# Kernel optimization log

Hardware: AMD Instinct MI355X
Metric: run time of the kernel (lower is better)

Reference implementation:

```python
import jax, jax.numpy as jnp
import numpy as np

E = 16        # n_experts
K = 2         # n_active_experts
D = 2048      # d_model
F = 1408      # ffn_hidden
B, S = 4, 2048


def _swiglu(x, wg, wu, wd):
    # x: [N, D]; wg/wu: [F, D]; wd: [D, F]
    return (jax.nn.silu(x @ wg.T) * (x @ wu.T)) @ wd.T


def setup_inputs() -> dict:
    key = jax.random.key(0)
    ks = jax.random.split(key, 8)
    sc = 0.02
    return {
        "x": jax.random.normal(ks[0], (B, S, D), jnp.float32),
        "gate_w": jax.random.normal(ks[1], (E, D), jnp.float32) * sc,
        "w_gate": jax.random.normal(ks[2], (E, F, D), jnp.float32) * sc,
        "w_up": jax.random.normal(ks[3], (E, F, D), jnp.float32) * sc,
        "w_down": jax.random.normal(ks[4], (E, D, F), jnp.float32) * sc,
        "sw_gate": jax.random.normal(ks[5], (F, D), jnp.float32) * sc,
        "sw_up": jax.random.normal(ks[6], (F, D), jnp.float32) * sc,
        "sw_down": jax.random.normal(ks[7], (D, F), jnp.float32) * sc,
        "expert_bias": jnp.zeros((E,), jnp.float32),
    }


def reference(x, gate_w, w_gate, w_up, w_down, sw_gate, sw_up, sw_down, expert_bias):
    b, s, d = x.shape
    flat = x.reshape(-1, d)                           # [N, D]
    logits = flat @ gate_w.T                          # [N, E]
    probs = jax.nn.softmax(logits, axis=-1)
    biased = logits + expert_bias
    _, top_idx = jax.lax.top_k(biased, K)             # [N, K] int32
    top_w = jnp.take_along_axis(probs, top_idx, axis=-1)
    top_w = top_w / jnp.sum(top_w, axis=-1, keepdims=True)
    # scatter top-k weights into a dense per-expert combine matrix [N, E]
    combine = jnp.sum(jax.nn.one_hot(top_idx, E, dtype=flat.dtype) * top_w[..., None], axis=1)
    out = jnp.zeros_like(flat)
    for e in range(E):  # fixed small expert loop
        out = out + combine[:, e:e + 1] * _swiglu(flat, w_gate[e], w_up[e], w_down[e])
    out = out + _swiglu(flat, sw_gate, sw_up, sw_down)  # shared expert
    return out.reshape(b, s, d)
```

## Files before the change

### kernel.cpp

```cpp
#include <hip/hip_runtime.h>
#include <hip/hip_bf16.h>
#include <cstdint>

#define NE 16
#define D_ 2048
#define F_ 1408
#define NTOK 8192
#define NPAIR (NTOK * 2)
#define SHARED_BASE NPAIR
#define NTOT (NPAIR + NTOK)

#define BM1 256
#define BN1 128
#define BN2 256
#define BK 64
#define NF1 (F_ / BN1)
#define NF2 (D_ / BN2)
#define MAXRT 111

typedef __attribute__((ext_vector_type(8))) short short8;
typedef __attribute__((ext_vector_type(4))) float f32x4;

static __device__ __forceinline__ ushort f2bf(float f) {
    union { float f; unsigned u; } v; v.f = f;
    unsigned u = v.u;
    return (ushort)((u + 0x7FFFu + ((u >> 16) & 1u)) >> 16);
}

static __device__ __forceinline__ float bf2f(ushort u) {
    union { unsigned u; float f; } v; v.u = ((unsigned)u) << 16;
    return v.f;
}

static __device__ __forceinline__ void cvt_store8(ushort* dst, const float* src) {
    const float4* s = reinterpret_cast<const float4*>(src);
    float4 a = s[0], b = s[1];
    short8 v;
    v[0] = (short)f2bf(a.x); v[1] = (short)f2bf(a.y);
    v[2] = (short)f2bf(a.z); v[3] = (short)f2bf(a.w);
    v[4] = (short)f2bf(b.x); v[5] = (short)f2bf(b.y);
    v[6] = (short)f2bf(b.z); v[7] = (short)f2bf(b.w);
    *reinterpret_cast<short8*>(dst) = v;
}

static __device__ __forceinline__ void gll16(const void* g, void* l) {
    __builtin_amdgcn_global_load_lds((const __attribute__((address_space(1))) void*)g,
                                     (__attribute__((address_space(3))) void*)l, 16, 0, 0);
}

static __device__ __forceinline__ int xcd_map(int p, int nwg) {
    int q = nwg >> 3, r = nwg & 7;
    int x = p & 7, k = p >> 3;
    int base = (x < r) ? x * (q + 1) : r * (q + 1) + (x - r) * q;
    return base + k;
}

__global__ __launch_bounds__(256) void k_cvt(const float* __restrict__ src,
                                             ushort* __restrict__ dst, int n8) {
    int i = blockIdx.x * 256 + threadIdx.x;
    int stride = gridDim.x * 256;
    for (; i < n8; i += stride) cvt_store8(dst + (size_t)i * 8, src + (size_t)i * 8);
}

__global__ __launch_bounds__(256) void k_route(const float* __restrict__ x,
                                               const float* __restrict__ gate_w,
                                               const float* __restrict__ expert_bias,
                                               int* __restrict__ topk_idx,
                                               float* __restrict__ topk_w) {
    const int wave = threadIdx.x >> 6;
    const int lane = threadIdx.x & 63;
    const int tok = blockIdx.x * 4 + wave;
    if (tok >= NTOK) return;
    const float* xr = x + (size_t)tok * D_;
    float xv[D_ / 64];
#pragma unroll
    for (int i = 0; i < D_ / 64; ++i) xv[i] = xr[lane + 64 * i];

    float logits[NE];
#pragma unroll
    for (int e = 0; e < NE; ++e) {
        const float* gw = gate_w + e * D_;
        float p = 0.f;
#pragma unroll
        for (int i = 0; i < D_ / 64; ++i) p += xv[i] * gw[lane + 64 * i];
#pragma unroll
        for (int off = 32; off > 0; off >>= 1) p += __shfl_xor(p, off, 64);
        logits[e] = p;
    }
    int i1 = 0; float b1 = logits[0] + expert_bias[0];
#pragma unroll
    for (int e = 1; e < NE; ++e) {
        float b = logits[e] + expert_bias[e];
        if (b > b1) { b1 = b; i1 = e; }
    }
    int i2 = -1; float b2 = -3.4e38f;
#pragma unroll
    for (int e = 0; e < NE; ++e) {
        if (e == i1) continue;
        float b = logits[e] + expert_bias[e];
        if (b > b2) { b2 = b; i2 = e; }
    }
    float l1 = logits[i1], l2 = logits[i2];
    float m = fmaxf(l1, l2);
    float e1 = __expf(l1 - m), e2 = __expf(l2 - m);
    float s = e1 + e2;
    if (lane == 0) {
        topk_idx[tok * 2 + 0] = i1;
        topk_idx[tok * 2 + 1] = i2;
        topk_w[tok * 2 + 0] = e1 / s;
        topk_w[tok * 2 + 1] = e2 / s;
    }
}

__global__ void k_zero_meta(int* meta) {
    if (threadIdx.x < 128) meta[threadIdx.x] = 0;
}

__global__ __launch_bounds__(256) void k_count(const int* __restrict__ topk_idx,
                                               int* __restrict__ meta) {
    int t = blockIdx.x * 256 + threadIdx.x;
    if (t >= NTOK) return;
    atomicAdd(&meta[topk_idx[t * 2 + 0]], 1);
    atomicAdd(&meta[topk_idx[t * 2 + 1]], 1);
}

__global__ void k_prefix(int* meta) {
    if (threadIdx.x == 0) {
        int acc = 0;
        for (int e = 0; e < NE; ++e) { meta[32 + e] = acc; acc += meta[e]; }
        meta[32 + NE] = acc;
        int t = 0;
        for (int e = 0; e < NE; ++e) { meta[64 + e] = t; t += (meta[e] + BM1 - 1) / BM1; }
        meta[64 + NE] = t;
        meta[64 + NE + 1] = t + NTOK / BM1;
    }
}

__global__ __launch_bounds__(256) void k_scatter(const int* __restrict__ topk_idx,
                                                 const float* __restrict__ topk_w,
                                                 int* __restrict__ meta,
                                                 int* __restrict__ tok_sorted,
                                                 float* __restrict__ w_sorted,
                                                 int* __restrict__ inv) {
    int t = blockIdx.x * 256 + threadIdx.x;
    if (t >= NTOK) return;
#pragma unroll
    for (int k = 0; k < 2; ++k) {
        int e = topk_idx[t * 2 + k];
        int p = atomicAdd(&meta[16 + e], 1);
        int idx = meta[32 + e] + p;
        tok_sorted[idx] = t;
        w_sorted[idx] = topk_w[t * 2 + k];
        inv[t * 2 + k] = idx;
    }
}

static __device__ __forceinline__ bool grid_decode(const int* meta, int bid, int NF,
                                                   int& e, int& row0, int& fx) {
    if (bid >= meta[64 + NE + 1] * NF) return false;
    e = (bid >= meta[64 + NE] * NF) ? NE : 0;
    if (e == 0) {
#pragma unroll
        for (int i = 1; i < NE; ++i) if (bid >= meta[64 + i] * NF) e = i;
    }
    const int tile_base = meta[64 + e];
    const int nrt = meta[64 + e + 1] - tile_base;
    const int bw = bid - tile_base * NF;
    fx = bw / nrt;
    row0 = (bw - fx * nrt) * BM1;
    return true;
}

__global__ __launch_bounds__(512, 2) void k_ffn1(const ushort* __restrict__ xb,
                                                 const ushort* __restrict__ wgb,
                                                 const ushort* __restrict__ wub,
                                                 const ushort* __restrict__ swgb,
                                                 const ushort* __restrict__ swub,
                                                 const int* __restrict__ meta,
                                                 const int* __restrict__ tok_sorted,
                                                 const float* __restrict__ w_sorted,
                                                 ushort* __restrict__ Hbuf) {
    int e, row0, fx;
    const int lbid = xcd_map(blockIdx.x, gridDim.x);
    if (!grid_decode(meta, lbid, NF1, e, row0, fx)) return;
    int n_e, base;
    if (e < NE) { n_e = meta[e]; base = meta[32 + e]; }
    else        { n_e = NTOK;    base = SHARED_BASE; }
    const int f0 = fx * BN1;
    const ushort* wg = (e < NE) ? wgb + (size_t)e * F_ * D_ : swgb;
    const ushort* wu = (e < NE) ? wub + (size_t)e * F_ * D_ : swub;

    __shared__ __align__(16) ushort As[2][BM1 * BK];
    __shared__ __align__(16) ushort Gs[2][BN1 * BK];
    __shared__ __align__(16) ushort Us[2][BN1 * BK];
    __shared__ int tks[BM1];
    __shared__ float tws[BM1];

    const int tid = threadIdx.x;
    const int wv = tid >> 6, lane = tid & 63;
    if (tid < BM1) {
        int r = row0 + tid;
        if (r < n_e) {
            tks[tid] = (e < NE) ? tok_sorted[base + r] : r;
            tws[tid] = (e < NE) ? w_sorted[base + r] : 1.0f;
        } else { tks[tid] = 0; tws[tid] = 0.f; }
    }
    __syncthreads();

    const ushort* srcA[4]; const ushort* srcG[2]; const ushort* srcU[2];
#pragma unroll
    for (int j = 0; j < 4; ++j) {
        int c = j * 512 + wv * 64 + lane;
        int r = c >> 3;
        int col = ((c & 7) ^ (r & 7)) * 8;
        srcA[j] = xb + (size_t)tks[r] * D_ + col;
    }
#pragma unroll
    for (int j = 0; j < 2; ++j) {
        int c = j * 512 + wv * 64 + lane;
        int r = c >> 3;
        int col = ((c & 7) ^ (r & 7)) * 8;
        srcG[j] = wg + (size_t)(f0 + r) * D_ + col;
        srcU[j] = wu + (size_t)(f0 + r) * D_ + col;
    }

    auto stage = [&](int buf, int k0) {
        char* bA = (char*)(&As[buf][0]) + wv * 1024;
        char* bG = (char*)(&Gs[buf][0]) + wv * 1024;
        char* bU = (char*)(&Us[buf][0]) + wv * 1024;
        gll16(srcA[0] + k0, bA);         gll16(srcA[1] + k0, bA + 8192);
        gll16(srcA[2] + k0, bA + 16384); gll16(srcA[3] + k0, bA + 24576);
        gll16(srcG[0] + k0, bG);         gll16(srcG[1] + k0, bG + 8192);
        gll16(srcU[0] + k0, bU);         gll16(srcU[1] + k0, bU + 8192);
    };

    f32x4 accg[4][4] = {}; f32x4 accu[4][4] = {};
    const int wm = (wv >> 1) * 64, wn = (wv & 1) * 64;
    const int fr = lane & 15, fq = lane >> 4;
    const int sw = fr & 7;
    const int rc0 = ((fq ^ sw) * 8);
    const int rc1 = (((4 + fq) ^ sw) * 8);

    auto compute = [&](int buf) {
        const ushort* pA = As[buf];
        const ushort* pG = Gs[buf];
        const ushort* pU = Us[buf];
#pragma unroll
        for (int kk = 0; kk < 2; ++kk) {
            const int rc = kk ? rc1 : rc0;
            short8 af[4], gf[4], uf[4];
#pragma unroll
            for (int mi = 0; mi < 4; ++mi)
                af[mi] = *reinterpret_cast<const short8*>(&pA[(wm + mi * 16 + fr) * BK + rc]);
#pragma unroll
            for (int ni = 0; ni < 4; ++ni) {
                gf[ni] = *reinterpret_cast<const short8*>(&pG[(wn + ni * 16 + fr) * BK + rc]);
                uf[ni] = *reinterpret_cast<const short8*>(&pU[(wn + ni * 16 + fr) * BK + rc]);
            }
#pragma unroll
            for (int mi = 0; mi < 4; ++mi)
#pragma unroll
                for (int ni = 0; ni < 4; ++ni) {
                    accg[mi][ni] = __builtin_amdgcn_mfma_f32_16x16x32_bf16(af[mi], gf[ni], accg[mi][ni], 0, 0, 0);
                    accu[mi][ni] = __builtin_amdgcn_mfma_f32_16x16x32_bf16(af[mi], uf[ni], accu[mi][ni], 0, 0, 0);
                }
        }
    };

    const int NK = D_ / BK;
    stage(0, 0);
    stage(1, BK);
    asm volatile("s_waitcnt vmcnt(8)" ::: "memory");
    __builtin_amdgcn_s_barrier();
    __builtin_amdgcn_sched_barrier(0);
    int cur = 0;
    for (int ks = 0; ks < NK; ++ks) {
        compute(cur);
        __builtin_amdgcn_s_barrier();
        if (ks + 2 < NK) {
            stage(cur, (ks + 2) * BK);
            asm volatile("s_waitcnt vmcnt(8)" ::: "memory");
        } else if (ks + 1 < NK) {
            asm volatile("s_waitcnt vmcnt(0)" ::: "memory");
        }
        __builtin_amdgcn_s_barrier();
        __builtin_amdgcn_sched_barrier(0);
        cur ^= 1;
    }

#pragma unroll
    for (int mi = 0; mi < 4; ++mi) {
#pragma unroll
        for (int r = 0; r < 4; ++r) {
            int lr = wm + mi * 16 + fq * 4 + r;
            int grow = row0 + lr;
            if (grow < n_e) {
                float w = tws[lr];
                ushort* hrow = Hbuf + (size_t)(base + grow) * F_ + f0 + wn;
#pragma unroll
                for (int ni = 0; ni < 4; ++ni) {
                    float g = accg[mi][ni][r];
                    float u = accu[mi][ni][r];
                    float h = w * (g / (1.f + __expf(-g))) * u;
                    hrow[ni * 16 + fr] = f2bf(h);
                }
            }
        }
    }
}

__global__ __launch_bounds__(512, 2) void k_ffn2(const ushort* __restrict__ Hbuf,
                                                 const ushort* __restrict__ wdb,
                                                 const ushort* __restrict__ swdb,
                                                 const int* __restrict__ meta,
                                                 ushort* __restrict__ Obuf) {
    int e, row0, dx;
    if (!grid_decode(meta, blockIdx.x, NF2, e, row0, dx)) return;
    int n_e, base;
    if (e < NE) { n_e = meta[e]; base = meta[32 + e]; }
    else        { n_e = NTOK;    base = SHARED_BASE; }
    const int d0 = dx * BN2;
    const ushort* wd = (e < NE) ? wdb + (size_t)e * D_ * F_ : swdb;

    __shared__ __align__(16) ushort As[2][BM1 * BK];
    __shared__ __align__(16) ushort Bs[2][BN2 * BK];

    const int tid = threadIdx.x;
    const int wv = tid >> 6, lane = tid & 63;

    const ushort* srcA[4]; const ushort* srcB[4];
#pragma unroll
    for (int j = 0; j < 4; ++j) {
        int c = j * 512 + wv * 64 + lane;
        int r = c >> 3;
        int col = ((c & 7) ^ (r & 7)) * 8;
        srcA[j] = Hbuf + (size_t)(base + row0 + r) * F_ + col;
        srcB[j] = wd + (size_t)(d0 + r) * F_ + col;
    }

    auto stage = [&](int buf, int k0) {
        char* bA = (char*)(&As[buf][0]) + wv * 1024;
        char* bB = (char*)(&Bs[buf][0]) + wv * 1024;
        gll16(srcA[0] + k0, bA);         gll16(srcA[1] + k0, bA + 8192);
        gll16(srcA[2] + k0, bA + 16384); gll16(srcA[3] + k0, bA + 24576);
        gll16(srcB[0] + k0, bB);         gll16(srcB[1] + k0, bB + 8192);
        gll16(srcB[2] + k0, bB + 16384); gll16(srcB[3] + k0, bB + 24576);
    };

    f32x4 acc[4][8] = {};
    const int wm = (wv >> 1) * 64, wn = (wv & 1) * 128;
    const int fr = lane & 15, fq = lane >> 4;
    const int sw = fr & 7;
    const int rc0 = ((fq ^ sw) * 8);
    const int rc1 = (((4 + fq) ^ sw) * 8);

    auto compute = [&](int buf) {
        const ushort* pA = As[buf];
        const ushort* pB = Bs[buf];
#pragma unroll
        for (int kk = 0; kk < 2; ++kk) {
            const int rc = kk ? rc1 : rc0;
            short8 af[4], bfr[8];
#pragma unroll
            for (int mi = 0; mi < 4; ++mi)
                af[mi] = *reinterpret_cast<const short8*>(&pA[(wm + mi * 16 + fr) * BK + rc]);
#pragma unroll
            for (int ni = 0; ni < 8; ++ni)
                bfr[ni] = *reinterpret_cast<const short8*>(&pB[(wn + ni * 16 + fr) * BK + rc]);
#pragma unroll
            for (int mi = 0; mi < 4; ++mi)
#pragma unroll
                for (int ni = 0; ni < 8; ++ni)
                    acc[mi][ni] = __builtin_amdgcn_mfma_f32_16x16x32_bf16(af[mi], bfr[ni], acc[mi][ni], 0, 0, 0);
        }
    };

    const int NK = F_ / BK;
    stage(0, 0);
    stage(1, BK);
    asm volatile("s_waitcnt vmcnt(8)" ::: "memory");
    __builtin_amdgcn_s_barrier();
    __builtin_amdgcn_sched_barrier(0);
    int cur = 0;
    for (int ks = 0; ks < NK; ++ks) {
        compute(cur);
        __builtin_amdgcn_s_barrier();
        if (ks + 2 < NK) {
            stage(cur, (ks + 2) * BK);
            asm volatile("s_waitcnt vmcnt(8)" ::: "memory");
        } else if (ks + 1 < NK) {
            asm volatile("s_waitcnt vmcnt(0)" ::: "memory");
        }
        __builtin_amdgcn_s_barrier();
        __builtin_amdgcn_sched_barrier(0);
        cur ^= 1;
    }

#pragma unroll
    for (int mi = 0; mi < 4; ++mi) {
#pragma unroll
        for (int r = 0; r < 4; ++r) {
            int lr = wm + mi * 16 + fq * 4 + r;
            int slot = row0 + lr;
            if (slot < n_e) {
                ushort* orow = Obuf + (size_t)(base + slot) * D_ + d0 + wn;
#pragma unroll
                for (int ni = 0; ni < 8; ++ni)
                    orow[ni * 16 + fr] = f2bf(acc[mi][ni][r]);
            }
        }
    }
}

__global__ __launch_bounds__(256) void k_gather(const ushort* __restrict__ Obuf,
                                                const int* __restrict__ inv,
                                                float* __restrict__ out) {
    const int t = blockIdx.x;
    const int c = threadIdx.x * 8;
    const int s1 = inv[t * 2 + 0];
    const int s2 = inv[t * 2 + 1];
    short8 a = *reinterpret_cast<const short8*>(&Obuf[(size_t)s1 * D_ + c]);
    short8 b = *reinterpret_cast<const short8*>(&Obuf[(size_t)s2 * D_ + c]);
    short8 d = *reinterpret_cast<const short8*>(&Obuf[(size_t)(SHARED_BASE + t) * D_ + c]);
    float4 o0, o1;
    o0.x = bf2f((ushort)a[0]) + bf2f((ushort)b[0]) + bf2f((ushort)d[0]);
    o0.y = bf2f((ushort)a[1]) + bf2f((ushort)b[1]) + bf2f((ushort)d[1]);
    o0.z = bf2f((ushort)a[2]) + bf2f((ushort)b[2]) + bf2f((ushort)d[2]);
    o0.w = bf2f((ushort)a[3]) + bf2f((ushort)b[3]) + bf2f((ushort)d[3]);
    o1.x = bf2f((ushort)a[4]) + bf2f((ushort)b[4]) + bf2f((ushort)d[4]);
    o1.y = bf2f((ushort)a[5]) + bf2f((ushort)b[5]) + bf2f((ushort)d[5]);
    o1.z = bf2f((ushort)a[6]) + bf2f((ushort)b[6]) + bf2f((ushort)d[6]);
    o1.w = bf2f((ushort)a[7]) + bf2f((ushort)b[7]) + bf2f((ushort)d[7]);
    float4* op = reinterpret_cast<float4*>(out + (size_t)t * D_ + c);
    op[0] = o0; op[1] = o1;
}

extern "C" void kernel_launch(void* const* d_in, const int* in_sizes, int n_in,
                              void* d_out, int out_size, void* d_ws, size_t ws_size,
                              hipStream_t stream) {
    const float* x        = (const float*)d_in[0];
    const float* gate_w   = (const float*)d_in[1];
    const float* w_gate   = (const float*)d_in[2];
    const float* w_up     = (const float*)d_in[3];
    const float* w_down   = (const float*)d_in[4];
    const float* sw_gate  = (const float*)d_in[5];
    const float* sw_up    = (const float*)d_in[6];
    const float* sw_down  = (const float*)d_in[7];
    const float* expert_bias = (const float*)d_in[8];
    float* out = (float*)d_out;

    const size_t NW = (size_t)NE * F_ * D_;
    const size_t NSW = (size_t)F_ * D_;
    const size_t NX = (size_t)NTOK * D_;

    char* ws = (char*)d_ws;
    size_t off = 0;
    ushort* xb   = (ushort*)(ws + off); off += NX * 2;
    ushort* wgb  = (ushort*)(ws + off); off += NW * 2;
    ushort* wub  = (ushort*)(ws + off); off += NW * 2;
    ushort* wdb  = (ushort*)(ws + off); off += NW * 2;
    ushort* swgb = (ushort*)(ws + off); off += NSW * 2;
    ushort* swub = (ushort*)(ws + off); off += NSW * 2;
    ushort* swdb = (ushort*)(ws + off); off += NSW * 2;
    ushort* Hbuf = (ushort*)(ws + off); off += (size_t)NTOT * F_ * 2;
    int* tok_sorted = (int*)(ws + off); off += NPAIR * sizeof(int);
    float* w_sorted = (float*)(ws + off); off += NPAIR * sizeof(float);
    int* topk_idx = (int*)(ws + off); off += NTOK * 2 * sizeof(int);
    float* topk_w = (float*)(ws + off); off += NTOK * 2 * sizeof(float);
    int* inv = (int*)(ws + off); off += NTOK * 2 * sizeof(int);
    int* meta = (int*)(ws + off); off += 512;

    ushort* Obuf = wgb;

    k_route<<<NTOK / 4, 256, 0, stream>>>(x, gate_w, expert_bias, topk_idx, topk_w);
    k_zero_meta<<<1, 128, 0, stream>>>(meta);
    k_count<<<NTOK / 256, 256, 0, stream>>>(topk_idx, meta);
    k_prefix<<<1, 1, 0, stream>>>(meta);
    k_scatter<<<NTOK / 256, 256, 0, stream>>>(topk_idx, topk_w, meta, tok_sorted, w_sorted, inv);

    auto cvt = [&](const float* s, ushort* d, size_t n) {
        int n8 = (int)(n / 8);
        int blocks = (n8 + 255) / 256;
        if (blocks > 4096) blocks = 4096;
        k_cvt<<<blocks, 256, 0, stream>>>(s, d, n8);
    };
    cvt(x, xb, NX);
    cvt(w_gate, wgb, NW);
    cvt(w_up, wub, NW);
    cvt(w_down, wdb, NW);
    cvt(sw_gate, swgb, NSW);
    cvt(sw_up, swub, NSW);
    cvt(sw_down, swdb, NSW);

    k_ffn1<<<MAXRT * NF1, 512, 0, stream>>>(xb, wgb, wub, swgb, swub,
                                            meta, tok_sorted, w_sorted, Hbuf);

    k_ffn2<<<MAXRT * NF2, 512, 0, stream>>>(Hbuf, wdb, swdb, meta, Obuf);

    k_gather<<<NTOK, 256, 0, stream>>>(Obuf, inv, out);
}
```

Baseline: 901.1 us.

## Overlap down-projection weight conversion with first FFN GEMM via extra blocks

```diff
diff --git a/kernel.cpp b/kernel.cpp
--- a/kernel.cpp
+++ b/kernel.cpp
@@ -17,6 +17,8 @@
 #define NF1 (F_ / BN1)
 #define NF2 (D_ / BN2)
 #define MAXRT 111
+#define GEMMB1 (MAXRT * NF1)
+#define CVTB 512
 
 typedef __attribute__((ext_vector_type(8))) short short8;
 typedef __attribute__((ext_vector_type(4))) float f32x4;
@@ -179,9 +181,29 @@
                                                  const int* __restrict__ meta,
                                                  const int* __restrict__ tok_sorted,
                                                  const float* __restrict__ w_sorted,
-                                                 ushort* __restrict__ Hbuf) {
+                                                 ushort* __restrict__ Hbuf,
+                                                 const float* __restrict__ w_down,
+                                                 const float* __restrict__ sw_down,
+                                                 ushort* __restrict__ wdb,
+                                                 ushort* __restrict__ swdb) {
+    const int tid = threadIdx.x;
+    if (blockIdx.x >= GEMMB1) {
+        const int NW8 = NE * F_ * D_ / 8;
+        const int NSW8 = F_ * D_ / 8;
+        int ci = (blockIdx.x - GEMMB1) * 512 + tid;
+        const int cstride = CVTB * 512;
+        for (; ci < NW8 + NSW8; ci += cstride) {
+            if (ci < NW8) cvt_store8(wdb + (size_t)ci * 8, w_down + (size_t)ci * 8);
+            else {
+                int j = ci - NW8;
+                cvt_store8(swdb + (size_t)j * 8, sw_down + (size_t)j * 8);
+            }
+        }
+        return;
+    }
+
     int e, row0, fx;
-    const int lbid = xcd_map(blockIdx.x, gridDim.x);
+    const int lbid = xcd_map(blockIdx.x, GEMMB1);
     if (!grid_decode(meta, lbid, NF1, e, row0, fx)) return;
     int n_e, base;
     if (e < NE) { n_e = meta[e]; base = meta[32 + e]; }
@@ -196,7 +218,6 @@
     __shared__ int tks[BM1];
     __shared__ float tws[BM1];
 
-    const int tid = threadIdx.x;
     const int wv = tid >> 6, lane = tid & 63;
     if (tid < BM1) {
         int r = row0 + tid;
@@ -487,13 +508,12 @@
     cvt(x, xb, NX);
     cvt(w_gate, wgb, NW);
     cvt(w_up, wub, NW);
-    cvt(w_down, wdb, NW);
     cvt(sw_gate, swgb, NSW);
     cvt(sw_up, swub, NSW);
-    cvt(sw_down, swdb, NSW);
-
-    k_ffn1<<<MAXRT * NF1, 512, 0, stream>>>(xb, wgb, wub, swgb, swub,
-                                            meta, tok_sorted, w_sorted, Hbuf);
+
+    k_ffn1<<<GEMMB1 + CVTB, 512, 0, stream>>>(xb, wgb, wub, swgb, swub,
+                                              meta, tok_sorted, w_sorted, Hbuf,
+                                              w_down, sw_down, wdb, swdb);
 
     k_ffn2<<<MAXRT * NF2, 512, 0, stream>>>(Hbuf, wdb, swdb, meta, Obuf);
 
```

After: 879.3 us. 2.4% less time.
